# Kernel tuning notes

Measured on AMD Instinct MI355X. Metric: run time of the kernel, lower is better.

Reference implementation:

```python
import jax, jax.numpy as jnp
import numpy as np

N_NODES = 100000
N_EDGES = 1600000
IN_FEATS, HIDDEN, OUT_MU, OUT_LV = 256, 128, 64, 64


def setup_inputs() -> dict:
    key = jax.random.key(0)
    ks = jax.random.split(key, 8)
    X = jax.random.normal(ks[0], (N_NODES, IN_FEATS), dtype=jnp.float32)
    edge_index = jax.random.randint(ks[1], (2, N_EDGES), 0, N_NODES, dtype=jnp.int64)
    def glorot(k, shape):
        lim = np.sqrt(6.0 / (shape[0] + shape[1])).astype(np.float32)
        return jax.random.uniform(k, shape, jnp.float32, -lim, lim)
    W1 = glorot(ks[2], (IN_FEATS, HIDDEN))
    b1 = jnp.zeros((HIDDEN,), jnp.float32)
    Wmu = glorot(ks[3], (HIDDEN, OUT_MU))
    bmu = jnp.zeros((OUT_MU,), jnp.float32)
    Wlv = glorot(ks[4], (HIDDEN, OUT_LV))
    blv = jnp.zeros((OUT_LV,), jnp.float32)
    return {"X": X, "edge_index": edge_index, "W1": W1, "b1": b1,
            "Wmu": Wmu, "bmu": bmu, "Wlv": Wlv, "blv": blv}


def _gcn_norm(edge_index, num_nodes):
    # Add self-loops (PyG GCNConv default) and compute symmetric normalization.
    loop = jnp.arange(num_nodes, dtype=edge_index.dtype)
    row = jnp.concatenate([edge_index[0], loop])  # source
    col = jnp.concatenate([edge_index[1], loop])  # target
    deg = jax.ops.segment_sum(jnp.ones_like(col, dtype=jnp.float32), col,
                              num_segments=num_nodes)
    dinv = jnp.where(deg > 0, jax.lax.rsqrt(deg), 0.0)
    norm = dinv[row] * dinv[col]  # [E+N]
    return row, col, norm


def _gcn_conv(x, W, b, row, col, norm, num_nodes):
    # Linear transform, then normalized sparse neighbor aggregation at targets.
    h = x @ W                                   # [N, F_out]
    msg = h[row] * norm[:, None]                # gather + scale, [E+N, F_out]
    out = jax.ops.segment_sum(msg, col, num_segments=num_nodes)
    return out + b


def reference(X, edge_index, W1, b1, Wmu, bmu, Wlv, blv):
    n = X.shape[0]
    row, col, norm = _gcn_norm(edge_index, n)
    H = jax.nn.relu(_gcn_conv(X, W1, b1, row, col, norm, n))
    mu = _gcn_conv(H, Wmu, bmu, row, col, norm, n)
    lv = _gcn_conv(H, Wlv, blv, row, col, norm, n)
    return (mu, lv)
```

## Files before the change

kernel.cpp:

```cpp
#include <hip/hip_runtime.h>
#include <hip/hip_bf16.h>
#include <cstdint>

#define N_FEATS_IN 256
#define HID 128
#define OUTF 64
#define SITEMS 8
#define NXCD 8

typedef __bf16 bf16x8 __attribute__((ext_vector_type(8)));
typedef __bf16 bf16x2 __attribute__((ext_vector_type(2)));
typedef float f32x4 __attribute__((ext_vector_type(4)));

__device__ __forceinline__ int xcc_id() {
  int x;
  asm volatile("s_getreg_b32 %0, hwreg(HW_REG_XCC_ID, 0, 32)" : "=s"(x));
  return x & (NXCD - 1);
}

__device__ __forceinline__ bf16x8 cvt8(float4 u, float4 v) {
  bf16x8 a;
  a[0] = (__bf16)u.x; a[1] = (__bf16)u.y; a[2] = (__bf16)u.z; a[3] = (__bf16)u.w;
  a[4] = (__bf16)v.x; a[5] = (__bf16)v.y; a[6] = (__bf16)v.z; a[7] = (__bf16)v.w;
  return a;
}


__global__ __launch_bounds__(256) void count_deg_kernel(const int* __restrict__ ei, int E,
    int N, int* __restrict__ cnt8, int* __restrict__ erank) {
  int e = blockIdx.x * 256 + threadIdx.x;
  int x = xcc_id();
  if (e < E) {
    int c = ei[E + e];
    int lr = __hip_atomic_fetch_add(&cnt8[(size_t)x * N + c], 1,
                                    __ATOMIC_RELAXED, __HIP_MEMORY_SCOPE_WORKGROUP);
    erank[e] = lr | (x << 28);
  }
}

__global__ __launch_bounds__(256) void combine_kernel(int* __restrict__ cnt8,
    int* __restrict__ deg, float* __restrict__ dinv, int n) {
  int c = blockIdx.x * 256 + threadIdx.x;
  if (c < n) {
    int s = 0;
#pragma unroll
    for (int x = 0; x < NXCD; ++x) {
      int v = cnt8[(size_t)x * n + c];
      cnt8[(size_t)x * n + c] = s;
      s += v;
    }
    deg[c] = s;
    dinv[c] = rsqrtf((float)(s + 1));
  }
}


__global__ __launch_bounds__(256) void scan_part_kernel(const int* __restrict__ cnt, int n,
                                                        int* __restrict__ bsum) {
  __shared__ int ts[256];
  const int t = threadIdx.x;
  int base = (blockIdx.x * 256 + t) * SITEMS;
  int s = 0;
#pragma unroll
  for (int i = 0; i < SITEMS; ++i) {
    int idx = base + i;
    if (idx < n) s += cnt[idx];
  }
  ts[t] = s;
  __syncthreads();
  for (int off = 128; off > 0; off >>= 1) {
    if (t < off) ts[t] += ts[t + off];
    __syncthreads();
  }
  if (t == 0) bsum[blockIdx.x] = ts[0];
}

__global__ __launch_bounds__(256) void scan_bsum_kernel(int* __restrict__ bsum, int nb) {
  __shared__ int ts[256];
  const int t = threadIdx.x;
  int v = (t < nb) ? bsum[t] : 0;
  ts[t] = v;
  __syncthreads();
  for (int off = 1; off < 256; off <<= 1) {
    int u = (t >= off) ? ts[t - off] : 0;
    __syncthreads();
    ts[t] += u;
    __syncthreads();
  }
  if (t < nb) bsum[t] = ts[t] - v;
}

__global__ __launch_bounds__(256) void scan_final_kernel(const int* __restrict__ cnt, int n,
    const int* __restrict__ bsum, int* __restrict__ ptr) {
  __shared__ int ts[256];
  const int t = threadIdx.x;
  int base = (blockIdx.x * 256 + t) * SITEMS;
  int loc[SITEMS];
  int s = 0;
#pragma unroll
  for (int i = 0; i < SITEMS; ++i) {
    int idx = base + i;
    loc[i] = (idx < n) ? cnt[idx] : 0;
    s += loc[i];
  }
  ts[t] = s;
  __syncthreads();
  for (int off = 1; off < 256; off <<= 1) {
    int u = (t >= off) ? ts[t - off] : 0;
    __syncthreads();
    ts[t] += u;
    __syncthreads();
  }
  int run = bsum[blockIdx.x] + ts[t] - s;
#pragma unroll
  for (int i = 0; i < SITEMS; ++i) {
    int idx = base + i;
    if (idx < n) ptr[idx] = run;
    run += loc[i];
  }
  if (base < n && base + SITEMS >= n) ptr[n] = run;
}


__global__ __launch_bounds__(256) void fill_kernel(const int* __restrict__ ei, int E, int N,
    const int* __restrict__ ptr, const int* __restrict__ offs, const int* __restrict__ erank,
    const float* __restrict__ dinv, int2* __restrict__ erec) {
  int e = blockIdx.x * 256 + threadIdx.x;
  if (e < E) {
    int r = ei[e];
    int c = ei[E + e];
    int er = erank[e];
    int x = er >> 28;
    int lr = er & 0x0FFFFFFF;
    int pos = ptr[c] + offs[(size_t)x * N + c] + lr;
    int2 rec;
    rec.x = r;
    rec.y = __float_as_int(dinv[r] * dinv[c]);
    erec[pos] = rec;
  }
}


__global__ __launch_bounds__(256) void pack_all_kernel(const float* __restrict__ W1,
    const float* __restrict__ Wmu, const float* __restrict__ Wlv,
    __bf16* __restrict__ W1p, __bf16* __restrict__ Wcp) {
  int idx = blockIdx.x * 256 + threadIdx.x;
  if (idx < 32768) {
    int j = idx & 7, l = (idx >> 3) & 63, t = (idx >> 9) & 7, s = idx >> 12;
    int k = s * 32 + (l >> 4) * 8 + j;
    int n = t * 16 + (l & 15);
    W1p[idx] = (__bf16)W1[k * HID + n];
  } else if (idx < 49152) {
    int i2 = idx - 32768;
    int j = i2 & 7, l = (i2 >> 3) & 63, t = (i2 >> 9) & 7, s = i2 >> 12;
    int k = s * 32 + (l >> 4) * 8 + j;
    int g = t * 16 + (l & 15);
    float v = (g < OUTF) ? Wmu[k * OUTF + g] : Wlv[k * OUTF + (g - OUTF)];
    Wcp[i2] = (__bf16)v;
  }
}


__global__ __launch_bounds__(256) void gemm1_mfma(const float* __restrict__ X,
    const __bf16* __restrict__ Wp, __bf16* __restrict__ Yb, int nrows, int ntiles) {
  __shared__ __bf16 bs[32768];
  const int tid = threadIdx.x;
  {
    const float4* s4 = (const float4*)Wp;
    float4* d4 = (float4*)bs;
#pragma unroll
    for (int i = 0; i < 16; ++i) d4[tid + 256 * i] = s4[tid + 256 * i];
  }
  __syncthreads();
  const int lane = tid & 63;
  const int wave = tid >> 6;
  const int lm = lane & 15;
  const int q = lane >> 4;
  const bf16x8* bsv = (const bf16x8*)bs;

  for (int tile = blockIdx.x; tile < ntiles; tile += gridDim.x) {
    const int row0 = tile * 64 + wave * 16;
    const int r = min(row0 + lm, nrows - 1);
    const float4* xp = (const float4*)(X + (size_t)r * N_FEATS_IN) + q * 2;

    float4 xa[16];
#pragma unroll
    for (int s = 0; s < 8; ++s) {
      xa[2 * s]     = xp[s * 8];
      xa[2 * s + 1] = xp[s * 8 + 1];
    }

    f32x4 acc[8];
#pragma unroll
    for (int t = 0; t < 8; ++t) acc[t] = (f32x4)0.f;

#pragma unroll
    for (int s = 0; s < 8; ++s) {
      bf16x8 a = cvt8(xa[2 * s], xa[2 * s + 1]);
#pragma unroll
      for (int t = 0; t < 8; ++t)
        acc[t] = __builtin_amdgcn_mfma_f32_16x16x32_bf16(a, bsv[(s * 8 + t) * 64 + lane],
                                                         acc[t], 0, 0, 0);
    }
#pragma unroll
    for (int t = 0; t < 8; ++t) {
#pragma unroll
      for (int r2 = 0; r2 < 4; ++r2) {
        int row = row0 + q * 4 + r2;
        if (row < nrows) Yb[(size_t)row * HID + t * 16 + lm] = (__bf16)acc[t][r2];
      }
    }
  }
}


__global__ __launch_bounds__(64) void agg_kernel(const __bf16* __restrict__ Fin,
    const int* __restrict__ ptr, const int2* __restrict__ erec,
    const float* __restrict__ dinv, const float* __restrict__ bias,
    __bf16* __restrict__ Fout, int do_relu) {
  const int c = blockIdx.x;
  const int t = threadIdx.x;
  const float d = dinv[c];
  bf16x2 sv = ((const bf16x2*)(Fin + (size_t)c * HID))[t];
  float ax = d * d * (float)sv[0];
  float ay = d * d * (float)sv[1];
  const int beg = ptr[c], end = ptr[c + 1];
  int e = beg;
  for (; e + 4 <= end; e += 4) {
    int2 p0 = erec[e], p1 = erec[e + 1], p2 = erec[e + 2], p3 = erec[e + 3];
    float n0 = __int_as_float(p0.y), n1 = __int_as_float(p1.y);
    float n2 = __int_as_float(p2.y), n3 = __int_as_float(p3.y);
    bf16x2 v0 = ((const bf16x2*)(Fin + (size_t)p0.x * HID))[t];
    bf16x2 v1 = ((const bf16x2*)(Fin + (size_t)p1.x * HID))[t];
    bf16x2 v2 = ((const bf16x2*)(Fin + (size_t)p2.x * HID))[t];
    bf16x2 v3 = ((const bf16x2*)(Fin + (size_t)p3.x * HID))[t];
    ax = fmaf(n0, (float)v0[0], ax); ay = fmaf(n0, (float)v0[1], ay);
    ax = fmaf(n1, (float)v1[0], ax); ay = fmaf(n1, (float)v1[1], ay);
    ax = fmaf(n2, (float)v2[0], ax); ay = fmaf(n2, (float)v2[1], ay);
    ax = fmaf(n3, (float)v3[0], ax); ay = fmaf(n3, (float)v3[1], ay);
  }
  for (; e < end; ++e) {
    int2 p = erec[e];
    float nn = __int_as_float(p.y);
    bf16x2 v = ((const bf16x2*)(Fin + (size_t)p.x * HID))[t];
    ax = fmaf(nn, (float)v[0], ax);
    ay = fmaf(nn, (float)v[1], ay);
  }
  if (do_relu) {
    ax = fmaxf(ax + bias[2 * t], 0.f);
    ay = fmaxf(ay + bias[2 * t + 1], 0.f);
  }
  bf16x2 o;
  o[0] = (__bf16)ax;
  o[1] = (__bf16)ay;
  ((bf16x2*)(Fout + (size_t)c * HID))[t] = o;
}


__global__ __launch_bounds__(256) void gemm2_mfma(const __bf16* __restrict__ Gb,
    const __bf16* __restrict__ Wp, const float* __restrict__ bmu,
    const float* __restrict__ blv, float* __restrict__ out, int nrows, int ntiles) {
  __shared__ __bf16 bs[16384];
  const int tid = threadIdx.x;
  {
    const float4* s4 = (const float4*)Wp;
    float4* d4 = (float4*)bs;
#pragma unroll
    for (int i = 0; i < 8; ++i) d4[tid + 256 * i] = s4[tid + 256 * i];
  }
  __syncthreads();
  const int lane = tid & 63;
  const int wave = tid >> 6;
  const int lm = lane & 15;
  const int q = lane >> 4;
  const bf16x8* bsv = (const bf16x8*)bs;

  const int g = (lane & 15) * 1;
  float bv[8];
  size_t obase[8];
#pragma unroll
  for (int t = 0; t < 8; ++t) {
    int col = t * 16 + (lane & 15);
    bv[t] = (col < OUTF) ? bmu[col] : blv[col - OUTF];
    obase[t] = (col < OUTF) ? (size_t)col : ((size_t)nrows * OUTF + (col - OUTF));
  }
  (void)g;

  for (int tile = blockIdx.x; tile < ntiles; tile += gridDim.x) {
    const int row0 = tile * 64 + wave * 16;
    const int r = min(row0 + lm, nrows - 1);
    const bf16x8* gp = (const bf16x8*)(Gb + (size_t)r * HID);

    bf16x8 xa[4];
#pragma unroll
    for (int s = 0; s < 4; ++s) xa[s] = gp[s * 4 + q];

    f32x4 acc[8];
#pragma unroll
    for (int t = 0; t < 8; ++t) acc[t] = (f32x4)0.f;

#pragma unroll
    for (int s = 0; s < 4; ++s) {
#pragma unroll
      for (int t = 0; t < 8; ++t)
        acc[t] = __builtin_amdgcn_mfma_f32_16x16x32_bf16(xa[s], bsv[(s * 8 + t) * 64 + lane],
                                                         acc[t], 0, 0, 0);
    }
#pragma unroll
    for (int t = 0; t < 8; ++t) {
#pragma unroll
      for (int r2 = 0; r2 < 4; ++r2) {
        int row = row0 + q * 4 + r2;
        if (row < nrows) out[obase[t] + (size_t)row * OUTF] = acc[t][r2] + bv[t];
      }
    }
  }
}


extern "C" void kernel_launch(void* const* d_in, const int* in_sizes, int n_in,
                              void* d_out, int out_size, void* d_ws, size_t ws_size,
                              hipStream_t stream) {
  const float* X   = (const float*)d_in[0];
  const int*   ei  = (const int*)d_in[1];
  const float* W1  = (const float*)d_in[2];
  const float* b1  = (const float*)d_in[3];
  const float* Wmu = (const float*)d_in[4];
  const float* bmu = (const float*)d_in[5];
  const float* Wlv = (const float*)d_in[6];
  const float* blv = (const float*)d_in[7];
  float* out = (float*)d_out;

  const int N = in_sizes[0] / N_FEATS_IN;
  const int E = in_sizes[1] / 2;

  char* ws = (char*)d_ws;
  size_t off = 0;
  auto alloc = [&](size_t bytes) -> void* {
    void* p = ws + off;
    off += (bytes + 255) & ~(size_t)255;
    return p;
  };
  __bf16* Yb  = (__bf16*)alloc((size_t)N * HID * 2);
  __bf16* Hb  = (__bf16*)alloc((size_t)N * HID * 2);
  float* dinv = (float*)alloc((size_t)N * 4);
  int*   deg  = (int*)alloc((size_t)N * 4);
  int*   ptr  = (int*)alloc((size_t)(N + 1) * 4);
  int*   cnt8 = (int*)alloc((size_t)NXCD * N * 4);
  int*   erank = (int*)alloc((size_t)E * 4);
  int2*  erec = (int2*)alloc((size_t)E * 8);
  __bf16* W1p = (__bf16*)alloc(32768 * 2);
  __bf16* Wcp = (__bf16*)alloc(16384 * 2);
  int*   bsum = (int*)alloc(256 * 4);
  (void)ws_size; (void)n_in; (void)out_size;

  hipMemsetAsync(cnt8, 0, (size_t)NXCD * N * 4, stream);

  int ge = (E + 255) / 256;
  int gn = (N + 255) / 256;
  int nb = (N + 256 * SITEMS - 1) / (256 * SITEMS);
  count_deg_kernel<<<ge, 256, 0, stream>>>(ei, E, N, cnt8, erank);
  combine_kernel<<<gn, 256, 0, stream>>>(cnt8, deg, dinv, N);
  scan_part_kernel<<<nb, 256, 0, stream>>>(deg, N, bsum);
  scan_bsum_kernel<<<1, 256, 0, stream>>>(bsum, nb);
  scan_final_kernel<<<nb, 256, 0, stream>>>(deg, N, bsum, ptr);
  fill_kernel<<<ge, 256, 0, stream>>>(ei, E, N, ptr, cnt8, erank, dinv, erec);
  pack_all_kernel<<<192, 256, 0, stream>>>(W1, Wmu, Wlv, W1p, Wcp);

  int ntiles = (N + 63) / 64;
  int g1 = ntiles < 512 ? ntiles : 512;
  int g2 = ntiles < 768 ? ntiles : 768;
  gemm1_mfma<<<g1, 256, 0, stream>>>(X, W1p, Yb, N, ntiles);
  agg_kernel<<<N, 64, 0, stream>>>(Yb, ptr, erec, dinv, b1, Hb, 1);
  agg_kernel<<<N, 64, 0, stream>>>(Hb, ptr, erec, dinv, b1, Yb, 0);
  gemm2_mfma<<<g2, 256, 0, stream>>>(Yb, Wcp, bmu, blv, out, N, ntiles);
}
```

Measured before the change: 460.2 us.

## Stage X tiles in LDS for gemm1 and deepen aggregation gather unroll

gemm1 now gives each block a 128-row tile. The block converts X to bf16 into padded shared memory, each wave computes two 16-row MFMA subtiles, and B fragments are read from global/L2 instead of a W copy in LDS. This drops the persistent grid-stride loop and the per-block load of the full weight into LDS, and reuses each B fragment across two row subtiles. The aggregation kernel adds an 8-wide unrolled loop to keep more independent row gathers in flight. Risks are higher register pressure and more global B reads per block.

Result: no change. 455.9 us (-0.9%).

```diff
diff --git a/kernel.cpp b/kernel.cpp
--- a/kernel.cpp
+++ b/kernel.cpp
@@ -7,8 +7,10 @@
 #define OUTF 64
 #define SITEMS 8
 #define NXCD 8
+#define XS_STRIDE 264
 
 typedef __bf16 bf16x8 __attribute__((ext_vector_type(8)));
+typedef __bf16 bf16x4 __attribute__((ext_vector_type(4)));
 typedef __bf16 bf16x2 __attribute__((ext_vector_type(2)));
 typedef float f32x4 __attribute__((ext_vector_type(4)));
 
@@ -16,13 +18,6 @@
   int x;
   asm volatile("s_getreg_b32 %0, hwreg(HW_REG_XCC_ID, 0, 32)" : "=s"(x));
   return x & (NXCD - 1);
-}
-
-__device__ __forceinline__ bf16x8 cvt8(float4 u, float4 v) {
-  bf16x8 a;
-  a[0] = (__bf16)u.x; a[1] = (__bf16)u.y; a[2] = (__bf16)u.z; a[3] = (__bf16)u.w;
-  a[4] = (__bf16)v.x; a[5] = (__bf16)v.y; a[6] = (__bf16)v.z; a[7] = (__bf16)v.w;
-  return a;
 }
 
 
@@ -120,7 +115,6 @@
   }
   if (base < n && base + SITEMS >= n) ptr[n] = run;
 }
-
 
 __global__ __launch_bounds__(256) void fill_kernel(const int* __restrict__ ei, int E, int N,
     const int* __restrict__ ptr, const int* __restrict__ offs, const int* __restrict__ erank,
@@ -162,52 +156,56 @@
 
 
 __global__ __launch_bounds__(256) void gemm1_mfma(const float* __restrict__ X,
-    const __bf16* __restrict__ Wp, __bf16* __restrict__ Yb, int nrows, int ntiles) {
-  __shared__ __bf16 bs[32768];
+    const __bf16* __restrict__ Wp, __bf16* __restrict__ Yb, int nrows) {
+  __shared__ __bf16 xs[128 * XS_STRIDE];
   const int tid = threadIdx.x;
-  {
-    const float4* s4 = (const float4*)Wp;
-    float4* d4 = (float4*)bs;
-#pragma unroll
-    for (int i = 0; i < 16; ++i) d4[tid + 256 * i] = s4[tid + 256 * i];
-  }
-  __syncthreads();
+  const int rowbase = blockIdx.x * 128;
+
+#pragma unroll
+  for (int i = 0; i < 32; ++i) {
+    int idx = i * 256 + tid;
+    int row = idx >> 6;
+    int cc = idx & 63;
+    int gr = min(rowbase + row, nrows - 1);
+    float4 v = ((const float4*)(X + (size_t)gr * N_FEATS_IN))[cc];
+    bf16x4 b;
+    b[0] = (__bf16)v.x; b[1] = (__bf16)v.y; b[2] = (__bf16)v.z; b[3] = (__bf16)v.w;
+    *(bf16x4*)(xs + row * XS_STRIDE + cc * 4) = b;
+  }
+  __syncthreads();
+
   const int lane = tid & 63;
   const int wave = tid >> 6;
   const int lm = lane & 15;
   const int q = lane >> 4;
-  const bf16x8* bsv = (const bf16x8*)bs;
-
-  for (int tile = blockIdx.x; tile < ntiles; tile += gridDim.x) {
-    const int row0 = tile * 64 + wave * 16;
-    const int r = min(row0 + lm, nrows - 1);
-    const float4* xp = (const float4*)(X + (size_t)r * N_FEATS_IN) + q * 2;
-
-    float4 xa[16];
-#pragma unroll
-    for (int s = 0; s < 8; ++s) {
-      xa[2 * s]     = xp[s * 8];
-      xa[2 * s + 1] = xp[s * 8 + 1];
-    }
-
-    f32x4 acc[8];
-#pragma unroll
-    for (int t = 0; t < 8; ++t) acc[t] = (f32x4)0.f;
-
-#pragma unroll
-    for (int s = 0; s < 8; ++s) {
-      bf16x8 a = cvt8(xa[2 * s], xa[2 * s + 1]);
-#pragma unroll
-      for (int t = 0; t < 8; ++t)
-        acc[t] = __builtin_amdgcn_mfma_f32_16x16x32_bf16(a, bsv[(s * 8 + t) * 64 + lane],
-                                                         acc[t], 0, 0, 0);
-    }
+  const bf16x8* wp = (const bf16x8*)Wp;
+
+  f32x4 acc[2][8];
+#pragma unroll
+  for (int m = 0; m < 2; ++m)
+#pragma unroll
+    for (int t = 0; t < 8; ++t) acc[m][t] = (f32x4)0.f;
+
+#pragma unroll
+  for (int s = 0; s < 8; ++s) {
+    bf16x8 a0 = *(const bf16x8*)(xs + (wave * 32 + lm) * XS_STRIDE + s * 32 + q * 8);
+    bf16x8 a1 = *(const bf16x8*)(xs + (wave * 32 + 16 + lm) * XS_STRIDE + s * 32 + q * 8);
 #pragma unroll
     for (int t = 0; t < 8; ++t) {
+      bf16x8 b = wp[(s * 8 + t) * 64 + lane];
+      acc[0][t] = __builtin_amdgcn_mfma_f32_16x16x32_bf16(a0, b, acc[0][t], 0, 0, 0);
+      acc[1][t] = __builtin_amdgcn_mfma_f32_16x16x32_bf16(a1, b, acc[1][t], 0, 0, 0);
+    }
+  }
+#pragma unroll
+  for (int m = 0; m < 2; ++m) {
+    int rb = rowbase + wave * 32 + m * 16 + q * 4;
+#pragma unroll
+    for (int t = 0; t < 8; ++t) {
 #pragma unroll
       for (int r2 = 0; r2 < 4; ++r2) {
-        int row = row0 + q * 4 + r2;
-        if (row < nrows) Yb[(size_t)row * HID + t * 16 + lm] = (__bf16)acc[t][r2];
+        int row = rb + r2;
+        if (row < nrows) Yb[(size_t)row * HID + t * 16 + lm] = (__bf16)acc[m][t][r2];
       }
     }
   }
@@ -226,14 +224,28 @@
   float ay = d * d * (float)sv[1];
   const int beg = ptr[c], end = ptr[c + 1];
   int e = beg;
+  for (; e + 8 <= end; e += 8) {
+    int2 p[8];
+#pragma unroll
+    for (int i = 0; i < 8; ++i) p[i] = erec[e + i];
+    bf16x2 v[8];
+#pragma unroll
+    for (int i = 0; i < 8; ++i) v[i] = ((const bf16x2*)(Fin + (size_t)p[i].x * HID))[t];
+#pragma unroll
+    for (int i = 0; i < 8; ++i) {
+      float nn = __int_as_float(p[i].y);
+      ax = fmaf(nn, (float)v[i][0], ax);
+      ay = fmaf(nn, (float)v[i][1], ay);
+    }
+  }
   for (; e + 4 <= end; e += 4) {
     int2 p0 = erec[e], p1 = erec[e + 1], p2 = erec[e + 2], p3 = erec[e + 3];
-    float n0 = __int_as_float(p0.y), n1 = __int_as_float(p1.y);
-    float n2 = __int_as_float(p2.y), n3 = __int_as_float(p3.y);
     bf16x2 v0 = ((const bf16x2*)(Fin + (size_t)p0.x * HID))[t];
     bf16x2 v1 = ((const bf16x2*)(Fin + (size_t)p1.x * HID))[t];
     bf16x2 v2 = ((const bf16x2*)(Fin + (size_t)p2.x * HID))[t];
     bf16x2 v3 = ((const bf16x2*)(Fin + (size_t)p3.x * HID))[t];
+    float n0 = __int_as_float(p0.y), n1 = __int_as_float(p1.y);
+    float n2 = __int_as_float(p2.y), n3 = __int_as_float(p3.y);
     ax = fmaf(n0, (float)v0[0], ax); ay = fmaf(n0, (float)v0[1], ay);
     ax = fmaf(n1, (float)v1[0], ax); ay = fmaf(n1, (float)v1[1], ay);
     ax = fmaf(n2, (float)v2[0], ax); ay = fmaf(n2, (float)v2[1], ay);
@@ -275,16 +287,14 @@
   const int q = lane >> 4;
   const bf16x8* bsv = (const bf16x8*)bs;
 
-  const int g = (lane & 15) * 1;
   float bv[8];
   size_t obase[8];
 #pragma unroll
   for (int t = 0; t < 8; ++t) {
-    int col = t * 16 + (lane & 15);
+    int col = t * 16 + lm;
     bv[t] = (col < OUTF) ? bmu[col] : blv[col - OUTF];
     obase[t] = (col < OUTF) ? (size_t)col : ((size_t)nrows * OUTF + (col - OUTF));
   }
-  (void)g;
 
   for (int tile = blockIdx.x; tile < ntiles; tile += gridDim.x) {
     const int row0 = tile * 64 + wave * 16;
@@ -367,11 +377,11 @@
   fill_kernel<<<ge, 256, 0, stream>>>(ei, E, N, ptr, cnt8, erank, dinv, erec);
   pack_all_kernel<<<192, 256, 0, stream>>>(W1, Wmu, Wlv, W1p, Wcp);
 
-  int ntiles = (N + 63) / 64;
-  int g1 = ntiles < 512 ? ntiles : 512;
-  int g2 = ntiles < 768 ? ntiles : 768;
-  gemm1_mfma<<<g1, 256, 0, stream>>>(X, W1p, Yb, N, ntiles);
+  int g1 = (N + 127) / 128;
+  gemm1_mfma<<<g1, 256, 0, stream>>>(X, W1p, Yb, N);
   agg_kernel<<<N, 64, 0, stream>>>(Yb, ptr, erec, dinv, b1, Hb, 1);
   agg_kernel<<<N, 64, 0, stream>>>(Hb, ptr, erec, dinv, b1, Yb, 0);
-  gemm2_mfma<<<g2, 256, 0, stream>>>(Yb, Wcp, bmu, blv, out, N, ntiles);
-}
+  int ntiles2 = (N + 63) / 64;
+  int g2 = ntiles2 < 768 ? ntiles2 : 768;
+  gemm2_mfma<<<g2, 256, 0, stream>>>(Yb, Wcp, bmu, blv, out, N, ntiles2);
+}
```
